# Kernel tuning notes

Hardware: AMD Instinct MI355X
Metric: run time of the kernel (lower is better)

The kernel has to match this reference:

```python
import jax, jax.numpy as jnp
import numpy as np

N = 100000   # nodes
IN = 256     # in_feats
OUT = 64     # out_feats per division
D = 4        # num_divisions (pairs=[], isFinal=False)
E = 800000   # edges per division


def setup_inputs() -> dict:
    key = jax.random.key(0)
    ks = jax.random.split(key, 6)
    feature = jax.random.normal(ks[0], (N, IN), jnp.float32)
    norm = jax.random.uniform(ks[1], (N, 1), jnp.float32)          # symmetric degree norm, positive
    W = jax.random.normal(ks[2], (D, IN, OUT), jnp.float32) * (1.0 / np.sqrt(IN))  # xavier-ish
    att_w = jax.random.normal(ks[3], (2 * OUT,), jnp.float32) * 0.1                # attention_linear weight
    src = jax.random.randint(ks[4], (D, E), 0, N, dtype=jnp.int32)
    dst = jax.random.randint(ks[5], (D, E), 0, N, dtype=jnp.int32)
    return {"feature": feature, "norm": norm, "W": W, "att_w": att_w, "src": src, "dst": dst}


def reference(feature, norm, W, att_w, src, dst):
    # dropout_prob = 0 -> all dropouts are identity (eval-mode reference).
    Nn = feature.shape[0]
    F = W.shape[-1]
    a_src, a_dst = att_w[:F], att_w[F:]
    outs = []
    for i in range(W.shape[0]):  # small fixed number of divisions (structurally distinct weights)
        s, d = src[i], dst[i]
        # per-division linear transform scaled by node norm: Wh_i = (h @ W_i) * norm
        Wh = (feature @ W[i]) * norm                       # [N, F]
        # GAT-style edge score: leaky_relu(att_w . [Wh_src ; Wh_dst])
        p_src = Wh @ a_src                                 # [N]
        p_dst = Wh @ a_dst                                 # [N]
        e = jax.nn.leaky_relu(p_src[s] + p_dst[d], negative_slope=0.2)  # [E]
        # edge softmax over incoming edges of each destination node
        m = jax.ops.segment_max(e, d, num_segments=Nn)     # [N], -inf for isolated dsts
        w = jnp.exp(e - m[d])                              # [E]
        z = jax.ops.segment_sum(w, d, num_segments=Nn)     # [N]
        a = w / z[d]                                       # [E] attention coefficients
        # weighted scatter-sum of source messages
        h_i = jax.ops.segment_sum(a[:, None] * Wh[s], d, num_segments=Nn)  # [N, F]
        outs.append(h_i)
    h_new = jnp.concatenate(outs, axis=-1) * norm          # merge='cat', then * norm
    return jax.nn.relu(h_new)                              # activation
```

## Files before the change

kernel.cpp:

```cpp
#include <hip/hip_runtime.h>

#define N_NODES 100000
#define IN_F    256
#define OUT_F   64
#define D_CH    4
#define N_EDGE  800000
#define M_SEG   (D_CH * N_NODES)
#define CPW     4

typedef __attribute__((ext_vector_type(8))) short short8;
typedef __attribute__((ext_vector_type(4))) float f32x4;

__device__ inline ushort f2bf(float f) {
    union { float f; unsigned u; } v; v.f = f;
    unsigned b = v.u + 0x7FFFu + ((v.u >> 16) & 1u);
    return (ushort)(b >> 16);
}
__device__ inline float bf2f(ushort u) {
    union { unsigned u; float f; } v; v.u = ((unsigned)u) << 16;
    return v.f;
}

__global__ __launch_bounds__(256) void bpack_kernel(
    const float* __restrict__ W, ushort* __restrict__ Bpack)
{
    const int t = blockIdx.x * 256 + threadIdx.x;
    if (t >= D_CH * 8 * 4 * 64) return;
    const int l  = t & 63;
    const int nt = (t >> 6) & 3;
    const int ks = (t >> 8) & 7;
    const int i  = t >> 11;
    const int n  = nt * 16 + (l & 15);
    const int k0 = ks * 32 + (l >> 4) * 8;
    ushort v[8];
#pragma unroll
    for (int j = 0; j < 8; ++j)
        v[j] = f2bf(W[((size_t)i * IN_F + k0 + j) * OUT_F + n]);
#pragma unroll
    for (int j = 0; j < 8; ++j)
        Bpack[(size_t)t * 8 + j] = v[j];
}

__global__ __launch_bounds__(256) void gemm_mfma_kernel(
    const float* __restrict__ feature, const float* __restrict__ norm,
    const ushort* __restrict__ Bpack, const float* __restrict__ att_w,
    ushort* __restrict__ Wh_b, float* __restrict__ p_src, float* __restrict__ p_dst)
{
    const int wv   = threadIdx.x >> 6;
    const int lane = threadIdx.x & 63;
    const int kg   = lane >> 4;
    const int cl   = lane & 15;
    const int r0   = blockIdx.x * 64 + wv * 16;

    const int rowm   = r0 + cl;
    const int rclamp = (rowm < N_NODES) ? rowm : (N_NODES - 1);
    const float* __restrict__ arow = feature + (size_t)rclamp * IN_F + kg * 8;
    short8 afrag[8];
#pragma unroll
    for (int ks = 0; ks < 8; ++ks) {
        const f32x4 x = *(const f32x4*)(arow + ks * 32);
        const f32x4 y = *(const f32x4*)(arow + ks * 32 + 4);
        short8 a;
        a[0] = (short)f2bf(x[0]); a[1] = (short)f2bf(x[1]);
        a[2] = (short)f2bf(x[2]); a[3] = (short)f2bf(x[3]);
        a[4] = (short)f2bf(y[0]); a[5] = (short)f2bf(y[1]);
        a[6] = (short)f2bf(y[2]); a[7] = (short)f2bf(y[3]);
        afrag[ks] = a;
    }

    float pa[4], pb[4];
#pragma unroll
    for (int nt = 0; nt < 4; ++nt) {
        pa[nt] = att_w[nt * 16 + cl];
        pb[nt] = att_w[OUT_F + nt * 16 + cl];
    }
    float nm[4];
    bool  rvld[4];
#pragma unroll
    for (int r = 0; r < 4; ++r) {
        const int rr = r0 + kg * 4 + r;
        rvld[r] = rr < N_NODES;
        nm[r] = rvld[r] ? norm[rr] : 0.f;
    }

    const short8* __restrict__ bp = (const short8*)Bpack;

    for (int i = 0; i < D_CH; ++i) {
        f32x4 acc[4];
#pragma unroll
        for (int nt = 0; nt < 4; ++nt) acc[nt] = (f32x4){0.f, 0.f, 0.f, 0.f};

#pragma unroll
        for (int ks = 0; ks < 8; ++ks) {
#pragma unroll
            for (int nt = 0; nt < 4; ++nt) {
                const short8 bf = bp[((((i * 8) + ks) * 4 + nt) << 6) + lane];
                acc[nt] = __builtin_amdgcn_mfma_f32_16x16x32_bf16(
                    afrag[ks], bf, acc[nt], 0, 0, 0);
            }
        }

        float ps[4] = {0.f, 0.f, 0.f, 0.f}, pd[4] = {0.f, 0.f, 0.f, 0.f};
#pragma unroll
        for (int nt = 0; nt < 4; ++nt) {
#pragma unroll
            for (int r = 0; r < 4; ++r) {
                const float v = acc[nt][r] * nm[r];
                const int rr = r0 + kg * 4 + r;
                if (rvld[r])
                    Wh_b[((size_t)i * N_NODES + rr) * OUT_F + nt * 16 + cl] = f2bf(v);
                ps[r] += v * pa[nt];
                pd[r] += v * pb[nt];
            }
        }
#pragma unroll
        for (int r = 0; r < 4; ++r) {
            float s1 = ps[r], s2 = pd[r];
#pragma unroll
            for (int off = 1; off < 16; off <<= 1) {
                s1 += __shfl_xor(s1, off, 64);
                s2 += __shfl_xor(s2, off, 64);
            }
            if (cl == 0 && rvld[r]) {
                const int rr = r0 + kg * 4 + r;
                p_src[i * N_NODES + rr] = s1;
                p_dst[i * N_NODES + rr] = s2;
            }
        }
    }
}

__global__ __launch_bounds__(256) void build_kernel(
    const int* __restrict__ src, const int* __restrict__ dst,
    int* __restrict__ head, int2* __restrict__ rec)
{
    const int e = blockIdx.x * 256 + threadIdx.x;
    const int i = blockIdx.y;
    const int d = dst[(size_t)i * N_EDGE + e];
    const int s = src[(size_t)i * N_EDGE + e];
    const int old = atomicExch(&head[i * N_NODES + d], e);
    rec[(size_t)i * N_EDGE + e] = make_int2(old, s);
}

__global__ __launch_bounds__(256) void agg_ll_kernel(
    const int* __restrict__ head, const int2* __restrict__ rec,
    const float* __restrict__ p_src, const float* __restrict__ p_dst,
    const ushort* __restrict__ Wh_b, const float* __restrict__ norm,
    float* __restrict__ out)
{
    const int wv   = threadIdx.x >> 6;
    const int lane = threadIdx.x & 63;
    const int g0   = (blockIdx.x * 4 + wv) * CPW;
    const int i  = g0 / N_NODES;
    const int n0 = g0 - i * N_NODES;

    const int2*   __restrict__ recb = rec + (size_t)i * N_EDGE;
    const float*  __restrict__ psb  = p_src + i * N_NODES;
    const ushort* __restrict__ whb  = Wh_b + (size_t)i * N_NODES * OUT_F + lane;

    int   vld[CPW], s[CPW], en[CPW];
    float pd[CPW], acc[CPW], z[CPW];
#pragma unroll
    for (int c = 0; c < CPW; ++c) {
        const int h = head[g0 + c];
        pd[c]  = p_dst[g0 + c];
        acc[c] = 0.f;
        z[c]   = 0.f;
        const int2 r = recb[(h >= 0) ? h : 0];
        vld[c] = (h >= 0);
        s[c]   = vld[c] ? r.y : 0;
        en[c]  = vld[c] ? r.x : -1;
    }

    for (;;) {
        int pending = 0;
#pragma unroll
        for (int c = 0; c < CPW; ++c) {
            const float ps = psb[s[c]];
            const float wh = bf2f(whb[(size_t)s[c] * OUT_F]);
            const int2  r  = recb[(en[c] >= 0) ? en[c] : 0];

            float x = ps + pd[c];
            x = (x > 0.f) ? x : 0.2f * x;
            float w = __expf(x);
            w = vld[c] ? w : 0.f;
            acc[c] += w * wh;
            z[c]   += w;

            const int live = (en[c] >= 0);
            vld[c] = live;
            s[c]   = live ? r.y : 0;
            en[c]  = live ? r.x : -1;
            pending |= live;
        }
        if (!pending) break;
    }

#pragma unroll
    for (int c = 0; c < CPW; ++c) {
        const int n = n0 + c;
        float v = (z[c] > 0.f) ? (acc[c] / z[c]) * norm[n] : 0.f;
        out[(size_t)n * (D_CH * OUT_F) + i * OUT_F + lane] = (v > 0.f) ? v : 0.f;
    }
}

extern "C" void kernel_launch(void* const* d_in, const int* in_sizes, int n_in,
                              void* d_out, int out_size, void* d_ws, size_t ws_size,
                              hipStream_t stream)
{
    const float* feature = (const float*)d_in[0];
    const float* norm    = (const float*)d_in[1];
    const float* W       = (const float*)d_in[2];
    const float* att_w   = (const float*)d_in[3];
    const int*   src     = (const int*)d_in[4];
    const int*   dst     = (const int*)d_in[5];
    float* out = (float*)d_out;

    ushort* Wh_b  = (ushort*)d_ws;
    float*  p_src = (float*)(Wh_b + (size_t)M_SEG * OUT_F);
    float*  p_dst = p_src + M_SEG;
    int*    head  = (int*)(p_dst + M_SEG);
    int2*   rec   = (int2*)(head + M_SEG);
    ushort* Bpack = (ushort*)(rec + (size_t)D_CH * N_EDGE);

    bpack_kernel<<<dim3(32), 256, 0, stream>>>(W, Bpack);
    gemm_mfma_kernel<<<dim3((N_NODES + 63) / 64), 256, 0, stream>>>(
        feature, norm, Bpack, att_w, Wh_b, p_src, p_dst);

    hipMemsetAsync(head, 0xFF, (size_t)M_SEG * sizeof(int), stream);
    build_kernel<<<dim3(N_EDGE / 256, D_CH), 256, 0, stream>>>(src, dst, head, rec);
    agg_ll_kernel<<<dim3(M_SEG / (4 * CPW)), 256, 0, stream>>>(
        head, rec, p_src, p_dst, Wh_b, norm, out);
}
```

Measured before the change: 441.0 us.

## Precompute edge attention weights in build pass and widen linked-list records

The edge score (leaky_relu plus exp of p_src[s]+p_dst[d]) now runs once per edge in the build kernel and is stored beside the next pointer and source index in a 16-byte record. The aggregation chain walk no longer needs a dependent p_src gather or the exp per step, only the record load and the Wh gather. Each wave also handles 8 chains instead of 4 for more memory-level parallelism. The trade-offs are a doubled record footprint and more registers per thread.

```diff
diff --git a/kernel.cpp b/kernel.cpp
--- a/kernel.cpp
+++ b/kernel.cpp
@@ -6,7 +6,7 @@
 #define D_CH    4
 #define N_EDGE  800000
 #define M_SEG   (D_CH * N_NODES)
-#define CPW     4
+#define CPW     8
 
 typedef __attribute__((ext_vector_type(8))) short short8;
 typedef __attribute__((ext_vector_type(4))) float f32x4;
@@ -19,6 +19,9 @@
 __device__ inline float bf2f(ushort u) {
     union { unsigned u; float f; } v; v.u = ((unsigned)u) << 16;
     return v.f;
+}
+__device__ inline float bits2f(int b) {
+    union { int i; float f; } v; v.i = b; return v.f;
 }
 
 __global__ __launch_bounds__(256) void bpack_kernel(
@@ -132,21 +135,25 @@
 
 __global__ __launch_bounds__(256) void build_kernel(
     const int* __restrict__ src, const int* __restrict__ dst,
-    int* __restrict__ head, int2* __restrict__ rec)
+    const float* __restrict__ p_src, const float* __restrict__ p_dst,
+    int* __restrict__ head, int4* __restrict__ rec)
 {
     const int e = blockIdx.x * 256 + threadIdx.x;
     const int i = blockIdx.y;
     const int d = dst[(size_t)i * N_EDGE + e];
     const int s = src[(size_t)i * N_EDGE + e];
+    float x = p_src[i * N_NODES + s] + p_dst[i * N_NODES + d];
+    x = (x > 0.f) ? x : 0.2f * x;
+    const float w = __expf(x);
+    union { float f; int i; } wb; wb.f = w;
     const int old = atomicExch(&head[i * N_NODES + d], e);
-    rec[(size_t)i * N_EDGE + e] = make_int2(old, s);
+    rec[(size_t)i * N_EDGE + e] = make_int4(old, s, wb.i, 0);
 }
 
 __global__ __launch_bounds__(256) void agg_ll_kernel(
-    const int* __restrict__ head, const int2* __restrict__ rec,
-    const float* __restrict__ p_src, const float* __restrict__ p_dst,
-    const ushort* __restrict__ Wh_b, const float* __restrict__ norm,
-    float* __restrict__ out)
+    const int* __restrict__ head, const int4* __restrict__ rec,
+    const float* __restrict__ p_dst_unused, const ushort* __restrict__ Wh_b,
+    const float* __restrict__ norm, float* __restrict__ out)
 {
     const int wv   = threadIdx.x >> 6;
     const int lane = threadIdx.x & 63;
@@ -154,43 +161,37 @@
     const int i  = g0 / N_NODES;
     const int n0 = g0 - i * N_NODES;
 
-    const int2*   __restrict__ recb = rec + (size_t)i * N_EDGE;
-    const float*  __restrict__ psb  = p_src + i * N_NODES;
+    const int4*   __restrict__ recb = rec + (size_t)i * N_EDGE;
     const ushort* __restrict__ whb  = Wh_b + (size_t)i * N_NODES * OUT_F + lane;
 
-    int   vld[CPW], s[CPW], en[CPW];
-    float pd[CPW], acc[CPW], z[CPW];
+    int   s[CPW], en[CPW];
+    float w[CPW], acc[CPW], z[CPW];
 #pragma unroll
     for (int c = 0; c < CPW; ++c) {
         const int h = head[g0 + c];
-        pd[c]  = p_dst[g0 + c];
+        const int4 r = recb[(h >= 0) ? h : 0];
+        const bool live = (h >= 0);
+        s[c]   = live ? r.y : 0;
+        w[c]   = live ? bits2f(r.z) : 0.f;
+        en[c]  = live ? r.x : -1;
         acc[c] = 0.f;
         z[c]   = 0.f;
-        const int2 r = recb[(h >= 0) ? h : 0];
-        vld[c] = (h >= 0);
-        s[c]   = vld[c] ? r.y : 0;
-        en[c]  = vld[c] ? r.x : -1;
     }
 
     for (;;) {
         int pending = 0;
 #pragma unroll
         for (int c = 0; c < CPW; ++c) {
-            const float ps = psb[s[c]];
-            const float wh = bf2f(whb[(size_t)s[c] * OUT_F]);
-            const int2  r  = recb[(en[c] >= 0) ? en[c] : 0];
-
-            float x = ps + pd[c];
-            x = (x > 0.f) ? x : 0.2f * x;
-            float w = __expf(x);
-            w = vld[c] ? w : 0.f;
-            acc[c] += w * wh;
-            z[c]   += w;
+            const float wh = bf2f(whb[(unsigned)(s[c] * OUT_F)]);
+            const int4  r  = recb[(en[c] >= 0) ? en[c] : 0];
+
+            acc[c] += w[c] * wh;
+            z[c]   += w[c];
 
             const int live = (en[c] >= 0);
-            vld[c] = live;
-            s[c]   = live ? r.y : 0;
-            en[c]  = live ? r.x : -1;
+            s[c]  = live ? r.y : 0;
+            w[c]  = live ? bits2f(r.z) : 0.f;
+            en[c] = live ? r.x : -1;
             pending |= live;
         }
         if (!pending) break;
@@ -220,7 +221,7 @@
     float*  p_src = (float*)(Wh_b + (size_t)M_SEG * OUT_F);
     float*  p_dst = p_src + M_SEG;
     int*    head  = (int*)(p_dst + M_SEG);
-    int2*   rec   = (int2*)(head + M_SEG);
+    int4*   rec   = (int4*)(head + M_SEG);
     ushort* Bpack = (ushort*)(rec + (size_t)D_CH * N_EDGE);
 
     bpack_kernel<<<dim3(32), 256, 0, stream>>>(W, Bpack);
@@ -228,7 +229,8 @@
         feature, norm, Bpack, att_w, Wh_b, p_src, p_dst);
 
     hipMemsetAsync(head, 0xFF, (size_t)M_SEG * sizeof(int), stream);
-    build_kernel<<<dim3(N_EDGE / 256, D_CH), 256, 0, stream>>>(src, dst, head, rec);
+    build_kernel<<<dim3(N_EDGE / 256, D_CH), 256, 0, stream>>>(
+        src, dst, p_src, p_dst, head, rec);
     agg_ll_kernel<<<dim3(M_SEG / (4 * CPW)), 256, 0, stream>>>(
-        head, rec, p_src, p_dst, Wh_b, norm, out);
-}
+        head, rec, p_dst, Wh_b, norm, out);
+}
```

After: 399.8 us. 1.1x faster.
